# Optimization experiments

Hardware: AMD Instinct MI355X
Metric: run time of the kernel (lower is better)

## Reference

```python
import jax, jax.numpy as jnp
import numpy as np

N = 20000          # nodes
DEG = 8            # deterministic in-degree per node
E = N * DEG        # edges
IN_DIM = 16
HID = 128
EDGE_DIM = 8
OUT_DIM = 4
LN_EPS = 1e-5
# degree histogram has all mass at DEG -> avg log-degree = log(DEG + 1)
AVG_DEG_LOG = float(np.log(DEG + 1.0))


def _init(key, fan_in, fan_out):
    s = float(np.sqrt(2.0 / (fan_in + fan_out)))  # glorot-ish
    return jax.random.normal(key, (fan_in, fan_out), jnp.float32) * s


def setup_inputs() -> dict:
    key = jax.random.key(0)
    ks = jax.random.split(key, 24)
    x = jax.random.normal(ks[0], (N, IN_DIM), jnp.float32)
    src = jax.random.randint(ks[1], (E,), 0, N, jnp.int32)
    dst = (jnp.arange(E, dtype=jnp.int32) % N)  # every node has exactly DEG in-edges
    edge_index = jnp.stack([src, dst], axis=0)
    edge_attr = jax.random.normal(ks[2], (E, EDGE_DIM), jnp.float32)
    d = {"x": x, "edge_attr": edge_attr, "edge_index": edge_index}
    i = 3
    for l, fi in enumerate([IN_DIM, HID]):  # 2 PNAConv layers (num_layers=3)
        d[f"ew{l}"] = _init(ks[i], EDGE_DIM, fi); i += 1   # edge_encoder
        d[f"eb{l}"] = jnp.zeros((fi,), jnp.float32)
        d[f"pw{l}"] = _init(ks[i], 3 * fi, fi); i += 1     # pre_nn: cat(x_i,x_j,e)
        d[f"pb{l}"] = jnp.zeros((fi,), jnp.float32)
        d[f"qw{l}"] = _init(ks[i], 13 * fi, HID); i += 1   # post_nn: (4 aggr * 3 scalers + 1)*F_in
        d[f"qb{l}"] = jnp.zeros((HID,), jnp.float32)
        d[f"lw{l}"] = _init(ks[i], HID, HID); i += 1       # PNAConv.lin
        d[f"lb{l}"] = jnp.zeros((HID,), jnp.float32)
        d[f"g{l}"] = jnp.ones((HID,), jnp.float32)         # LayerNorm gamma
        d[f"b{l}"] = jnp.zeros((HID,), jnp.float32)        # LayerNorm beta
    d["hw"] = _init(ks[i], HID, OUT_DIM)
    d["hb"] = jnp.zeros((OUT_DIM,), jnp.float32)
    return d


def _pna_conv(x, src, dst, edge_attr, ew, eb, pw, pb, qw, qb, lw, lb):
    # messages: cat(x_i, x_j, edge_encoder(edge_attr)) -> pre MLP
    e = edge_attr @ ew + eb                                   # [E, F_in]
    h = jnp.concatenate([x[dst], x[src], e], axis=-1)         # [E, 3*F_in]
    h = h @ pw + pb                                           # [E, F_in]
    # multi-aggregator reduce by destination node
    deg = jax.ops.segment_sum(jnp.ones((E,), h.dtype), dst, num_segments=N)
    degc = jnp.maximum(deg, 1.0)[:, None]
    mean = jax.ops.segment_sum(h, dst, num_segments=N) / degc
    mean2 = jax.ops.segment_sum(h * h, dst, num_segments=N) / degc
    mx = jax.ops.segment_max(h, dst, num_segments=N)
    mn = jax.ops.segment_min(h, dst, num_segments=N)
    std = jnp.sqrt(jax.nn.relu(mean2 - mean * mean) + 1e-5)
    agg = jnp.concatenate([mean, mx, mn, std], axis=-1)       # [N, 4*F_in]
    # degree scalers: identity, amplification, attenuation (scaler-major layout)
    logd = jnp.log(deg + 1.0)[:, None]
    scaled = jnp.concatenate(
        [agg, agg * (logd / AVG_DEG_LOG), agg * (AVG_DEG_LOG / logd)], axis=-1
    )                                                         # [N, 12*F_in]
    out = jnp.concatenate([x, scaled], axis=-1) @ qw + qb     # post_nn, [N, F_out]
    return out @ lw + lb                                      # PNAConv.lin


def _ln(x, g, b):
    m = jnp.mean(x, axis=-1, keepdims=True)
    v = jnp.mean((x - m) ** 2, axis=-1, keepdims=True)
    return (x - m) / jnp.sqrt(v + LN_EPS) * g + b


def reference(x, edge_attr, ew0, eb0, pw0, pb0, qw0, qb0, lw0, lb0, g0, b0,
              ew1, eb1, pw1, pb1, qw1, qb1, lw1, lb1, g1, b1, hw, hb, edge_index):
    src, dst = edge_index[0], edge_index[1]
    h = _pna_conv(x, src, dst, edge_attr, ew0, eb0, pw0, pb0, qw0, qb0, lw0, lb0)
    h = jax.nn.relu(_ln(h, g0, b0))  # dropout is identity at inference
    h = _pna_conv(h, src, dst, edge_attr, ew1, eb1, pw1, pb1, qw1, qb1, lw1, lb1)
    h = jax.nn.relu(_ln(h, g1, b1))
    return h @ hw + hb               # head, [N, OUT_DIM]
```

## Files before the change

kernel.cpp:

```cpp
#include <hip/hip_runtime.h>
#include <math.h>

#define N_NODES 20000
#define N_EDGES 160000

typedef unsigned short ushort_t;
typedef __attribute__((ext_vector_type(8))) short short8v;
typedef __attribute__((ext_vector_type(4))) float f32x4;

#define WS_We0  0
#define WS_b0m  128
#define WS_W0   256
#define WS_b0   10496
#define WS_We1  10624
#define WS_b1m  11648
#define WS_W1   11776
#define WS_b1   93696
#define WS_WP1  93824
#define WS_WPTU 134784
#define WS_t0   151168
#define WS_u0   471168
#define WS_A0   791168
#define WS_A1   151168
#define WS_h0b  5271296
#define WS_t1   6551296
#define WS_u1   9111296

__device__ inline ushort_t f2bf(float f) {
    union { float f; unsigned u; } v; v.f = f;
    unsigned r = v.u + 0x7FFFu + ((v.u >> 16) & 1u);
    return (ushort_t)(r >> 16);
}

__global__ __launch_bounds__(256) void k_prep(
    const float* __restrict__ x,
    const float* __restrict__ ew0, const float* __restrict__ eb0,
    const float* __restrict__ pw0, const float* __restrict__ pb0,
    const float* __restrict__ qw0, const float* __restrict__ qb0,
    const float* __restrict__ lw0, const float* __restrict__ lb0,
    const float* __restrict__ ew1, const float* __restrict__ eb1,
    const float* __restrict__ pw1, const float* __restrict__ pb1,
    const float* __restrict__ qw1, const float* __restrict__ qb1,
    const float* __restrict__ lw1, const float* __restrict__ lb1,
    float* __restrict__ ws)
{
    int tid = blockIdx.x * 256 + threadIdx.x;
    if (tid < 81920) {
        int r = tid >> 7, o = tid & 127;
        float acc = 0.f;
        for (int h = 0; h < 128; ++h) {
            float qr;
            if (r < 128) qr = qw1[r*128 + h];
            else {
                int s = r - 128;
                qr = qw1[(128+s)*128+h] + qw1[(640+s)*128+h] + qw1[(1152+s)*128+h];
            }
            acc += qr * lw1[h*128 + o];
        }
        ws[WS_W1 + tid] = acc;
    } else if (tid < 82048) {
        int o = tid - 81920;
        float acc = lb1[o];
        for (int h = 0; h < 128; ++h) acc += qb1[h] * lw1[h*128 + o];
        ws[WS_b1 + o] = acc;
    } else if (tid < 92288) {
        int idx = tid - 82048; int r = idx >> 7, o = idx & 127;
        float acc = 0.f;
        for (int h = 0; h < 128; ++h) {
            float qr;
            if (r < 16) qr = qw0[r*128 + h];
            else {
                int s = r - 16;
                qr = qw0[(16+s)*128+h] + qw0[(80+s)*128+h] + qw0[(144+s)*128+h];
            }
            acc += qr * lw0[h*128 + o];
        }
        ws[WS_W0 + idx] = acc;
    } else if (tid < 92416) {
        int o = tid - 92288;
        float acc = lb0[o];
        for (int h = 0; h < 128; ++h) acc += qb0[h] * lw0[h*128 + o];
        ws[WS_b0 + o] = acc;
    } else if (tid < 93440) {
        int idx = tid - 92416; int c = idx >> 7, f = idx & 127;
        float acc = 0.f;
        for (int k = 0; k < 128; ++k) acc += ew1[c*128 + k] * pw1[(256+k)*128 + f];
        ws[WS_We1 + idx] = acc;
    } else if (tid < 93568) {
        int f = tid - 93440;
        float acc = pb1[f];
        for (int k = 0; k < 128; ++k) acc += eb1[k] * pw1[(256+k)*128 + f];
        ws[WS_b1m + f] = acc;
    } else if (tid < 93696) {
        int idx = tid - 93568; int c = idx >> 4, f = idx & 15;
        float acc = 0.f;
        for (int k = 0; k < 16; ++k) acc += ew0[c*16 + k] * pw0[(32+k)*16 + f];
        ws[WS_We0 + idx] = acc;
    } else if (tid < 93712) {
        int f = tid - 93696;
        float acc = pb0[f];
        for (int k = 0; k < 16; ++k) acc += eb0[k] * pw0[(32+k)*16 + f];
        ws[WS_b0m + f] = acc;
    } else if (tid < 413712) {
        int idx = tid - 93712; int i = idx >> 4, f = idx & 15;
        float acc = 0.f;
        for (int k = 0; k < 16; ++k) acc += x[i*16 + k] * pw0[k*16 + f];
        ws[WS_t0 + idx] = acc;
    } else if (tid < 733712) {
        int idx = tid - 413712; int i = idx >> 4, f = idx & 15;
        float acc = 0.f;
        for (int k = 0; k < 16; ++k) acc += x[i*16 + k] * pw0[(16+k)*16 + f];
        ws[WS_u0 + idx] = acc;
    }
}

__global__ __launch_bounds__(256) void k_pack(
    const float* __restrict__ pw1, float* __restrict__ ws)
{
    int tid = blockIdx.x * 256 + threadIdx.x;
    if (tid < 10240) {
        ushort_t* WP1 = (ushort_t*)(ws + WS_WP1);
        const float* W1f = ws + WS_W1;
        int l = tid & 63, ctks = tid >> 6;
        int ct = ctks / 20, ks = ctks % 20;
        int col = ct*16 + (l & 15);
        int k0 = ks*32 + (l >> 4)*8;
        short8v v;
        #pragma unroll
        for (int j = 0; j < 8; ++j) v[j] = (short)f2bf(W1f[(k0+j)*128 + col]);
        *(short8v*)(WP1 + (size_t)tid*8) = v;
    } else if (tid < 14336) {
        int idx = tid - 10240;
        ushort_t* WPT = (ushort_t*)(ws + WS_WPTU);
        int l = idx & 63, ctks = idx >> 6;
        int ct = ctks >> 2, ks = ctks & 3;
        int base_k = (ct < 8) ? 0 : 128;
        int col = (ct & 7)*16 + (l & 15);
        int k0 = base_k + ks*32 + (l >> 4)*8;
        short8v v;
        #pragma unroll
        for (int j = 0; j < 8; ++j) v[j] = (short)f2bf(pw1[(k0+j)*128 + col]);
        *(short8v*)(WPT + (size_t)idx*8) = v;
    }
}

__global__ __launch_bounds__(256) void k_agg0(
    const float* __restrict__ x, const float* __restrict__ ea,
    const int* __restrict__ src, float* __restrict__ ws)
{
    __shared__ float ea_s[16*8*8];
    __shared__ int   src_s[16*8];
    __shared__ float We0_s[128];
    __shared__ float b0m_s[16];
    const int t = threadIdx.x;
    const int i0 = blockIdx.x * 16;

    for (int idx = t; idx < 1024; idx += 256) {
        int k = idx >> 7; int rem = idx & 127; int n = rem >> 3, c = rem & 7;
        ea_s[(n*8 + k)*8 + c] = ea[(i0 + n + k*N_NODES)*8 + c];
    }
    if (t < 128) {
        int k = t >> 4, n = t & 15;
        src_s[n*8 + k] = src[i0 + n + k*N_NODES];
        We0_s[t] = ws[WS_We0 + t];
    }
    if (t < 16) b0m_s[t] = ws[WS_b0m + t];
    __syncthreads();

    const int n = t >> 4, f = t & 15;
    const int i = i0 + n;
    float base = ws[WS_t0 + i*16 + f] + b0m_s[f];
    float s = 0.f, q = 0.f, mx = -1e30f, mn = 1e30f;
    for (int k = 0; k < 8; ++k) {
        int sj = src_s[n*8 + k];
        float m = base + ws[WS_u0 + sj*16 + f];
        #pragma unroll
        for (int c = 0; c < 8; ++c) m += ea_s[(n*8+k)*8 + c] * We0_s[c*16 + f];
        s += m; q += m*m; mx = fmaxf(mx, m); mn = fminf(mn, m);
    }
    float mean = s * 0.125f, mean2 = q * 0.125f;
    float sd = sqrtf(fmaxf(mean2 - mean*mean, 0.f) + 1e-5f);
    float* A0 = ws + WS_A0 + (size_t)i * 80;
    A0[f]      = x[i*16 + f];
    A0[16 + f] = mean;
    A0[32 + f] = mx;
    A0[48 + f] = mn;
    A0[64 + f] = sd;
}

__global__ __launch_bounds__(256) void k_gemm0(
    const float* __restrict__ g0, const float* __restrict__ bln0,
    float* __restrict__ ws)
{
    __shared__ float As[32][81];
    const int t = threadIdx.x;
    const int r0 = blockIdx.x * 32;
    const float* A = ws + WS_A0 + (size_t)r0 * 80;
    for (int idx = t; idx < 32*80; idx += 256) {
        int r = idx / 80, k = idx - r*80;
        As[r][k] = A[idx];
    }
    __syncthreads();
    const int tc = t & 31, tr = t >> 5;
    const int c0 = tc * 4;
    float acc[4][4] = {};
    const float* W = ws + WS_W0;
    #pragma unroll 4
    for (int k = 0; k < 80; ++k) {
        float4 b = *(const float4*)(W + k*128 + c0);
        #pragma unroll
        for (int rr = 0; rr < 4; ++rr) {
            float a = As[tr*4 + rr][k];
            acc[rr][0] += a*b.x; acc[rr][1] += a*b.y;
            acc[rr][2] += a*b.z; acc[rr][3] += a*b.w;
        }
    }
    float4 bias = *(const float4*)(ws + WS_b0 + c0);
    float4 g  = *(const float4*)(g0 + c0);
    float4 bb = *(const float4*)(bln0 + c0);
    ushort_t* h0b = (ushort_t*)(ws + WS_h0b);
    #pragma unroll
    for (int rr = 0; rr < 4; ++rr) {
        float v0 = acc[rr][0] + bias.x, v1 = acc[rr][1] + bias.y;
        float v2 = acc[rr][2] + bias.z, v3 = acc[rr][3] + bias.w;
        float sum = v0+v1+v2+v3;
        float sq  = v0*v0+v1*v1+v2*v2+v3*v3;
        #pragma unroll
        for (int off = 1; off < 32; off <<= 1) {
            sum += __shfl_xor(sum, off, 64);
            sq  += __shfl_xor(sq,  off, 64);
        }
        float mean = sum * (1.f/128.f);
        float var  = sq  * (1.f/128.f) - mean*mean;
        float rstd = rsqrtf(var + 1e-5f);
        ushort4 ob;
        ob.x = f2bf(fmaxf((v0-mean)*rstd*g.x + bb.x, 0.f));
        ob.y = f2bf(fmaxf((v1-mean)*rstd*g.y + bb.y, 0.f));
        ob.z = f2bf(fmaxf((v2-mean)*rstd*g.z + bb.z, 0.f));
        ob.w = f2bf(fmaxf((v3-mean)*rstd*g.w + bb.w, 0.f));
        *(ushort4*)(h0b + (size_t)(r0 + tr*4 + rr)*128 + c0) = ob;
    }
}

__global__ __launch_bounds__(64) void k_tu1(float* __restrict__ ws)
{
    const int lane = threadIdx.x;
    const int rowbase = blockIdx.x * 16;
    const ushort_t* h0b = (const ushort_t*)(ws + WS_h0b);
    const ushort_t* WP  = (const ushort_t*)(ws + WS_WPTU);
    const int lr = lane & 15, lk = lane >> 4;
    const size_t arow = rowbase + lr;
    f32x4 acc[16];
    #pragma unroll
    for (int c = 0; c < 16; ++c) acc[c] = (f32x4){0.f,0.f,0.f,0.f};

    #pragma unroll
    for (int ks = 0; ks < 4; ++ks) {
        short8v a = *(const short8v*)(h0b + arow*128 + ks*32 + lk*8);
        #pragma unroll
        for (int c = 0; c < 16; ++c) {
            short8v b = *(const short8v*)(WP + ((size_t)(c*4 + ks)*64 + lane)*8);
            acc[c] = __builtin_amdgcn_mfma_f32_16x16x32_bf16(a, b, acc[c], 0, 0, 0);
        }
    }
    float* t1 = ws + WS_t1;
    float* u1 = ws + WS_u1;
    #pragma unroll
    for (int c = 0; c < 16; ++c) {
        float* dst = (c < 8) ? t1 : u1;
        int cb = (c & 7)*16 + lr;
        #pragma unroll
        for (int r = 0; r < 4; ++r) {
            int row = rowbase + lk*4 + r;
            dst[(size_t)row*128 + cb] = acc[c][r];
        }
    }
}

__global__ __launch_bounds__(256) void k_agg1(
    const float* __restrict__ ea, const int* __restrict__ src,
    float* __restrict__ ws)
{
    __shared__ float ea_s[16*8*8];
    __shared__ int   src_s[128];
    __shared__ float We1_s[1024];
    __shared__ float b1m_s[128];
    const int t = threadIdx.x;
    const int i0 = blockIdx.x * 16;

    for (int idx = t; idx < 1024; idx += 256) {
        int k = idx >> 7; int rem = idx & 127; int n = rem >> 3, c = rem & 7;
        ea_s[(n*8 + k)*8 + c] = ea[(i0 + n + k*N_NODES)*8 + c];
    }
    if (t < 128) {
        int k = t >> 4, n = t & 15;
        src_s[n*8 + k] = src[i0 + n + k*N_NODES];
    }
    for (int idx = t; idx < 1024; idx += 256) We1_s[idx] = ws[WS_We1 + idx];
    if (t < 128) b1m_s[t] = ws[WS_b1m + t];
    __syncthreads();

    const int n = t >> 4, f0 = (t & 15) * 8;
    const int i = i0 + n;
    float base[8], sm[8], sq[8], mx[8], mn[8];
    #pragma unroll
    for (int e = 0; e < 8; ++e) {
        base[e] = ws[WS_t1 + (size_t)i*128 + f0 + e] + b1m_s[f0 + e];
        sm[e] = 0.f; sq[e] = 0.f; mx[e] = -1e30f; mn[e] = 1e30f;
    }
    for (int k = 0; k < 8; ++k) {
        int sj = src_s[n*8 + k];
        const float* urow = ws + WS_u1 + (size_t)sj*128 + f0;
        float m[8];
        #pragma unroll
        for (int e = 0; e < 8; ++e) m[e] = base[e] + urow[e];
        #pragma unroll
        for (int c = 0; c < 8; ++c) {
            float a = ea_s[(n*8 + k)*8 + c];
            #pragma unroll
            for (int e = 0; e < 8; ++e) m[e] += a * We1_s[c*128 + f0 + e];
        }
        #pragma unroll
        for (int e = 0; e < 8; ++e) {
            sm[e] += m[e]; sq[e] += m[e]*m[e];
            mx[e] = fmaxf(mx[e], m[e]); mn[e] = fminf(mn[e], m[e]);
        }
    }
    ushort_t* A1 = (ushort_t*)(ws + WS_A1);
    short8v vm, vx, vn, vs;
    #pragma unroll
    for (int e = 0; e < 8; ++e) {
        float mean = sm[e]*0.125f, m2 = sq[e]*0.125f;
        float sd = sqrtf(fmaxf(m2 - mean*mean, 0.f) + 1e-5f);
        vm[e] = (short)f2bf(mean);
        vx[e] = (short)f2bf(mx[e]);
        vn[e] = (short)f2bf(mn[e]);
        vs[e] = (short)f2bf(sd);
    }
    size_t b = (size_t)i*512 + f0;
    *(short8v*)(A1 + b)       = vm;
    *(short8v*)(A1 + b + 128) = vx;
    *(short8v*)(A1 + b + 256) = vn;
    *(short8v*)(A1 + b + 384) = vs;
}

__global__ __launch_bounds__(64) void k_gemm1(
    const float* __restrict__ g1, const float* __restrict__ bln1,
    const float* __restrict__ hw, const float* __restrict__ hb,
    float* __restrict__ ws, float* __restrict__ out)
{
    const int lane = threadIdx.x;
    const int rowbase = blockIdx.x * 16;
    const ushort_t* h0b = (const ushort_t*)(ws + WS_h0b);
    const ushort_t* A1  = (const ushort_t*)(ws + WS_A1);
    const ushort_t* WP  = (const ushort_t*)(ws + WS_WP1);
    const int lr = lane & 15, lk = lane >> 4;
    const size_t arow = rowbase + lr;

    f32x4 acc[8];
    #pragma unroll
    for (int c = 0; c < 8; ++c) acc[c] = (f32x4){0.f,0.f,0.f,0.f};

    #pragma unroll
    for (int ks = 0; ks < 4; ++ks) {
        short8v a = *(const short8v*)(h0b + arow*128 + ks*32 + lk*8);
        #pragma unroll
        for (int c = 0; c < 8; ++c) {
            short8v b = *(const short8v*)(WP + ((size_t)(c*20 + ks)*64 + lane)*8);
            acc[c] = __builtin_amdgcn_mfma_f32_16x16x32_bf16(a, b, acc[c], 0, 0, 0);
        }
    }
    #pragma unroll 4
    for (int ks = 0; ks < 16; ++ks) {
        short8v a = *(const short8v*)(A1 + arow*512 + ks*32 + lk*8);
        #pragma unroll
        for (int c = 0; c < 8; ++c) {
            short8v b = *(const short8v*)(WP + ((size_t)(c*20 + 4 + ks)*64 + lane)*8);
            acc[c] = __builtin_amdgcn_mfma_f32_16x16x32_bf16(a, b, acc[c], 0, 0, 0);
        }
    }

    float bc[8], gc[8], bbc[8]; f32x4 hwc[8];
    #pragma unroll
    for (int c = 0; c < 8; ++c) {
        int col = c*16 + lr;
        bc[c]  = ws[WS_b1 + col];
        gc[c]  = g1[col];
        bbc[c] = bln1[col];
        hwc[c] = *(const f32x4*)(hw + col*4);
    }
    f32x4 hb4 = *(const f32x4*)hb;
    #pragma unroll
    for (int r = 0; r < 4; ++r) {
        float v[8]; float s = 0.f, q = 0.f;
        #pragma unroll
        for (int c = 0; c < 8; ++c) {
            v[c] = acc[c][r] + bc[c];
            s += v[c]; q += v[c]*v[c];
        }
        #pragma unroll
        for (int off = 1; off < 16; off <<= 1) {
            s += __shfl_xor(s, off, 64);
            q += __shfl_xor(q, off, 64);
        }
        float mean = s * (1.f/128.f);
        float var  = q * (1.f/128.f) - mean*mean;
        float rstd = rsqrtf(var + 1e-5f);
        f32x4 po = (f32x4){0.f,0.f,0.f,0.f};
        #pragma unroll
        for (int c = 0; c < 8; ++c) {
            float o = fmaxf((v[c]-mean)*rstd*gc[c] + bbc[c], 0.f);
            po += o * hwc[c];
        }
        #pragma unroll
        for (int off = 1; off < 16; off <<= 1) {
            po.x += __shfl_xor(po.x, off, 64);
            po.y += __shfl_xor(po.y, off, 64);
            po.z += __shfl_xor(po.z, off, 64);
            po.w += __shfl_xor(po.w, off, 64);
        }
        if (lr == 0) {
            int row = rowbase + lk*4 + r;
            f32x4 res = po + hb4;
            *(f32x4*)(out + (size_t)row*4) = res;
        }
    }
}

extern "C" void kernel_launch(void* const* d_in, const int* in_sizes, int n_in,
                              void* d_out, int out_size, void* d_ws, size_t ws_size,
                              hipStream_t stream)
{
    const float* x    = (const float*)d_in[0];
    const float* ea   = (const float*)d_in[1];
    const int*   eidx = (const int*)d_in[2];
    const float* ew0  = (const float*)d_in[3];
    const float* eb0  = (const float*)d_in[4];
    const float* pw0  = (const float*)d_in[5];
    const float* pb0  = (const float*)d_in[6];
    const float* qw0  = (const float*)d_in[7];
    const float* qb0  = (const float*)d_in[8];
    const float* lw0  = (const float*)d_in[9];
    const float* lb0  = (const float*)d_in[10];
    const float* g0   = (const float*)d_in[11];
    const float* bl0  = (const float*)d_in[12];
    const float* ew1  = (const float*)d_in[13];
    const float* eb1  = (const float*)d_in[14];
    const float* pw1  = (const float*)d_in[15];
    const float* pb1  = (const float*)d_in[16];
    const float* qw1  = (const float*)d_in[17];
    const float* qb1  = (const float*)d_in[18];
    const float* lw1  = (const float*)d_in[19];
    const float* lb1  = (const float*)d_in[20];
    const float* g1   = (const float*)d_in[21];
    const float* bl1  = (const float*)d_in[22];
    const float* hw   = (const float*)d_in[23];
    const float* hb   = (const float*)d_in[24];
    const int* src = eidx;
    float* ws = (float*)d_ws;
    float* out = (float*)d_out;

    k_prep<<<2867, 256, 0, stream>>>(x, ew0, eb0, pw0, pb0, qw0, qb0, lw0, lb0,
                                     ew1, eb1, pw1, pb1, qw1, qb1, lw1, lb1, ws);
    k_pack<<<56, 256, 0, stream>>>(pw1, ws);
    k_agg0<<<1250, 256, 0, stream>>>(x, ea, src, ws);
    k_gemm0<<<625, 256, 0, stream>>>(g0, bl0, ws);
    k_tu1<<<1250, 64, 0, stream>>>(ws);
    k_agg1<<<1250, 256, 0, stream>>>(ea, src, ws);
    k_gemm1<<<1250, 64, 0, stream>>>(g1, bl1, hw, hb, ws, out);
}
```

Baseline: 108.6 us.

## Fuse layer-1 aggregation into post-GEMM and pack weights directly in prep

The layer-1 aggregation kernel and the following MFMA GEMM kernel become one kernel. Each lane computes mean/max/min/std statistics for its row and feature slice in registers and feeds them straight into the MFMA A operands, so the bf16 aggregate buffer is never written to or read back from global memory. The separate weight-pack kernel is also removed: the prep kernel writes the bf16 MFMA-layout weights directly, which saves a launch and the fp32 intermediate. In exchange, each 64-thread block now does the gathers with lower parallelism and higher register pressure than the former 256-thread aggregation kernel.

```diff
diff --git a/kernel.cpp b/kernel.cpp
--- a/kernel.cpp
+++ b/kernel.cpp
@@ -7,6 +7,7 @@
 typedef unsigned short ushort_t;
 typedef __attribute__((ext_vector_type(8))) short short8v;
 typedef __attribute__((ext_vector_type(4))) float f32x4;
+typedef __attribute__((ext_vector_type(8))) float f32x8;
 
 #define WS_We0  0
 #define WS_b0m  128
@@ -14,17 +15,15 @@
 #define WS_b0   10496
 #define WS_We1  10624
 #define WS_b1m  11648
-#define WS_W1   11776
-#define WS_b1   93696
-#define WS_WP1  93824
-#define WS_WPTU 134784
-#define WS_t0   151168
-#define WS_u0   471168
-#define WS_A0   791168
-#define WS_A1   151168
-#define WS_h0b  5271296
-#define WS_t1   6551296
-#define WS_u1   9111296
+#define WS_b1   11776
+#define WS_WP1  11904
+#define WS_WPTU 52864
+#define WS_t0   69248
+#define WS_u0   389248
+#define WS_h0b  709248
+#define WS_t1   1989248
+#define WS_u1   4549248
+#define WS_A0   7109248
 
 __device__ inline ushort_t f2bf(float f) {
     union { float f; unsigned u; } v; v.f = f;
@@ -57,7 +56,9 @@
             }
             acc += qr * lw1[h*128 + o];
         }
-        ws[WS_W1 + tid] = acc;
+        int ct = o >> 4, ks = r >> 5;
+        int l = (o & 15) | (((r >> 3) & 3) << 4);
+        ((ushort_t*)(ws + WS_WP1))[(size_t)(((ct*20 + ks)*64) + l)*8 + (r & 7)] = f2bf(acc);
     } else if (tid < 82048) {
         int o = tid - 81920;
         float acc = lb1[o];
@@ -101,46 +102,24 @@
         float acc = pb0[f];
         for (int k = 0; k < 16; ++k) acc += eb0[k] * pw0[(32+k)*16 + f];
         ws[WS_b0m + f] = acc;
-    } else if (tid < 413712) {
-        int idx = tid - 93712; int i = idx >> 4, f = idx & 15;
+    } else if (tid < 126480) {
+        int idx = tid - 93712;
+        int r = idx >> 7, o = idx & 127;
+        int part = r >> 7, rk = r & 127;
+        int ct = part*8 + (o >> 4);
+        int l = (o & 15) | (((rk >> 3) & 3) << 4);
+        ((ushort_t*)(ws + WS_WPTU))[(size_t)(((ct*4 + (rk >> 5))*64) + l)*8 + (rk & 7)]
+            = f2bf(pw1[r*128 + o]);
+    } else if (tid < 446480) {
+        int idx = tid - 126480; int i = idx >> 4, f = idx & 15;
         float acc = 0.f;
         for (int k = 0; k < 16; ++k) acc += x[i*16 + k] * pw0[k*16 + f];
         ws[WS_t0 + idx] = acc;
-    } else if (tid < 733712) {
-        int idx = tid - 413712; int i = idx >> 4, f = idx & 15;
+    } else if (tid < 766480) {
+        int idx = tid - 446480; int i = idx >> 4, f = idx & 15;
         float acc = 0.f;
         for (int k = 0; k < 16; ++k) acc += x[i*16 + k] * pw0[(16+k)*16 + f];
         ws[WS_u0 + idx] = acc;
-    }
-}
-
-__global__ __launch_bounds__(256) void k_pack(
-    const float* __restrict__ pw1, float* __restrict__ ws)
-{
-    int tid = blockIdx.x * 256 + threadIdx.x;
-    if (tid < 10240) {
-        ushort_t* WP1 = (ushort_t*)(ws + WS_WP1);
-        const float* W1f = ws + WS_W1;
-        int l = tid & 63, ctks = tid >> 6;
-        int ct = ctks / 20, ks = ctks % 20;
-        int col = ct*16 + (l & 15);
-        int k0 = ks*32 + (l >> 4)*8;
-        short8v v;
-        #pragma unroll
-        for (int j = 0; j < 8; ++j) v[j] = (short)f2bf(W1f[(k0+j)*128 + col]);
-        *(short8v*)(WP1 + (size_t)tid*8) = v;
-    } else if (tid < 14336) {
-        int idx = tid - 10240;
-        ushort_t* WPT = (ushort_t*)(ws + WS_WPTU);
-        int l = idx & 63, ctks = idx >> 6;
-        int ct = ctks >> 2, ks = ctks & 3;
-        int base_k = (ct < 8) ? 0 : 128;
-        int col = (ct & 7)*16 + (l & 15);
-        int k0 = base_k + ks*32 + (l >> 4)*8;
-        short8v v;
-        #pragma unroll
-        for (int j = 0; j < 8; ++j) v[j] = (short)f2bf(pw1[(k0+j)*128 + col]);
-        *(short8v*)(WPT + (size_t)idx*8) = v;
     }
 }
 
@@ -277,106 +256,90 @@
     }
 }
 
-__global__ __launch_bounds__(256) void k_agg1(
+__global__ __launch_bounds__(64) void k_fuse1(
     const float* __restrict__ ea, const int* __restrict__ src,
-    float* __restrict__ ws)
-{
-    __shared__ float ea_s[16*8*8];
-    __shared__ int   src_s[128];
-    __shared__ float We1_s[1024];
-    __shared__ float b1m_s[128];
-    const int t = threadIdx.x;
-    const int i0 = blockIdx.x * 16;
-
-    for (int idx = t; idx < 1024; idx += 256) {
-        int k = idx >> 7; int rem = idx & 127; int n = rem >> 3, c = rem & 7;
-        ea_s[(n*8 + k)*8 + c] = ea[(i0 + n + k*N_NODES)*8 + c];
-    }
-    if (t < 128) {
-        int k = t >> 4, n = t & 15;
-        src_s[n*8 + k] = src[i0 + n + k*N_NODES];
-    }
-    for (int idx = t; idx < 1024; idx += 256) We1_s[idx] = ws[WS_We1 + idx];
-    if (t < 128) b1m_s[t] = ws[WS_b1m + t];
-    __syncthreads();
-
-    const int n = t >> 4, f0 = (t & 15) * 8;
-    const int i = i0 + n;
-    float base[8], sm[8], sq[8], mx[8], mn[8];
-    #pragma unroll
-    for (int e = 0; e < 8; ++e) {
-        base[e] = ws[WS_t1 + (size_t)i*128 + f0 + e] + b1m_s[f0 + e];
-        sm[e] = 0.f; sq[e] = 0.f; mx[e] = -1e30f; mn[e] = 1e30f;
-    }
-    for (int k = 0; k < 8; ++k) {
-        int sj = src_s[n*8 + k];
-        const float* urow = ws + WS_u1 + (size_t)sj*128 + f0;
-        float m[8];
-        #pragma unroll
-        for (int e = 0; e < 8; ++e) m[e] = base[e] + urow[e];
-        #pragma unroll
-        for (int c = 0; c < 8; ++c) {
-            float a = ea_s[(n*8 + k)*8 + c];
-            #pragma unroll
-            for (int e = 0; e < 8; ++e) m[e] += a * We1_s[c*128 + f0 + e];
-        }
-        #pragma unroll
-        for (int e = 0; e < 8; ++e) {
-            sm[e] += m[e]; sq[e] += m[e]*m[e];
-            mx[e] = fmaxf(mx[e], m[e]); mn[e] = fminf(mn[e], m[e]);
-        }
-    }
-    ushort_t* A1 = (ushort_t*)(ws + WS_A1);
-    short8v vm, vx, vn, vs;
-    #pragma unroll
-    for (int e = 0; e < 8; ++e) {
-        float mean = sm[e]*0.125f, m2 = sq[e]*0.125f;
-        float sd = sqrtf(fmaxf(m2 - mean*mean, 0.f) + 1e-5f);
-        vm[e] = (short)f2bf(mean);
-        vx[e] = (short)f2bf(mx[e]);
-        vn[e] = (short)f2bf(mn[e]);
-        vs[e] = (short)f2bf(sd);
-    }
-    size_t b = (size_t)i*512 + f0;
-    *(short8v*)(A1 + b)       = vm;
-    *(short8v*)(A1 + b + 128) = vx;
-    *(short8v*)(A1 + b + 256) = vn;
-    *(short8v*)(A1 + b + 384) = vs;
-}
-
-__global__ __launch_bounds__(64) void k_gemm1(
     const float* __restrict__ g1, const float* __restrict__ bln1,
     const float* __restrict__ hw, const float* __restrict__ hb,
     float* __restrict__ ws, float* __restrict__ out)
 {
     const int lane = threadIdx.x;
+    const int lr = lane & 15, lk = lane >> 4;
     const int rowbase = blockIdx.x * 16;
+    const int row = rowbase + lr;
     const ushort_t* h0b = (const ushort_t*)(ws + WS_h0b);
-    const ushort_t* A1  = (const ushort_t*)(ws + WS_A1);
     const ushort_t* WP  = (const ushort_t*)(ws + WS_WP1);
-    const int lr = lane & 15, lk = lane >> 4;
-    const size_t arow = rowbase + lr;
+
+    int sj[8];
+    #pragma unroll
+    for (int e = 0; e < 8; ++e) sj[e] = src[row + e*N_NODES];
 
     f32x4 acc[8];
     #pragma unroll
     for (int c = 0; c < 8; ++c) acc[c] = (f32x4){0.f,0.f,0.f,0.f};
 
     #pragma unroll
-    for (int ks = 0; ks < 4; ++ks) {
-        short8v a = *(const short8v*)(h0b + arow*128 + ks*32 + lk*8);
+    for (int kw = 0; kw < 4; ++kw) {
+        short8v a = *(const short8v*)(h0b + (size_t)row*128 + kw*32 + lk*8);
         #pragma unroll
         for (int c = 0; c < 8; ++c) {
-            short8v b = *(const short8v*)(WP + ((size_t)(c*20 + ks)*64 + lane)*8);
+            short8v b = *(const short8v*)(WP + (size_t)((c*20 + kw)*64 + lane)*8);
             acc[c] = __builtin_amdgcn_mfma_f32_16x16x32_bf16(a, b, acc[c], 0, 0, 0);
         }
     }
-    #pragma unroll 4
-    for (int ks = 0; ks < 16; ++ks) {
-        short8v a = *(const short8v*)(A1 + arow*512 + ks*32 + lk*8);
-        #pragma unroll
-        for (int c = 0; c < 8; ++c) {
-            short8v b = *(const short8v*)(WP + ((size_t)(c*20 + 4 + ks)*64 + lane)*8);
-            acc[c] = __builtin_amdgcn_mfma_f32_16x16x32_bf16(a, b, acc[c], 0, 0, 0);
+
+    #pragma unroll
+    for (int q = 0; q < 4; ++q) {
+        const int f0 = q*32 + lk*8;
+        f32x8 wv[8];
+        #pragma unroll
+        for (int c = 0; c < 8; ++c)
+            wv[c] = *(const f32x8*)(ws + WS_We1 + c*128 + f0);
+        f32x8 t1v  = *(const f32x8*)(ws + WS_t1 + (size_t)row*128 + f0);
+        f32x8 b1m8 = *(const f32x8*)(ws + WS_b1m + f0);
+        float base[8], sm[8], sq[8], mx[8], mn[8];
+        #pragma unroll
+        for (int j = 0; j < 8; ++j) {
+            base[j] = t1v[j] + b1m8[j];
+            sm[j] = 0.f; sq[j] = 0.f; mx[j] = -1e30f; mn[j] = 1e30f;
+        }
+        #pragma unroll
+        for (int e = 0; e < 8; ++e) {
+            f32x8 uv = *(const f32x8*)(ws + WS_u1 + (size_t)sj[e]*128 + f0);
+            f32x8 av = *(const f32x8*)(ea + (size_t)(row + e*N_NODES)*8);
+            float m[8];
+            #pragma unroll
+            for (int j = 0; j < 8; ++j) m[j] = base[j] + uv[j];
+            #pragma unroll
+            for (int c = 0; c < 8; ++c) {
+                #pragma unroll
+                for (int j = 0; j < 8; ++j) m[j] += av[c] * wv[c][j];
+            }
+            #pragma unroll
+            for (int j = 0; j < 8; ++j) {
+                sm[j] += m[j]; sq[j] += m[j]*m[j];
+                mx[j] = fmaxf(mx[j], m[j]); mn[j] = fminf(mn[j], m[j]);
+            }
+        }
+        float stat[4][8];
+        #pragma unroll
+        for (int j = 0; j < 8; ++j) {
+            float mean = sm[j]*0.125f, m2 = sq[j]*0.125f;
+            stat[0][j] = mean;
+            stat[1][j] = mx[j];
+            stat[2][j] = mn[j];
+            stat[3][j] = sqrtf(fmaxf(m2 - mean*mean, 0.f) + 1e-5f);
+        }
+        #pragma unroll
+        for (int agg = 0; agg < 4; ++agg) {
+            short8v a;
+            #pragma unroll
+            for (int j = 0; j < 8; ++j) a[j] = (short)f2bf(stat[agg][j]);
+            const int ks = agg*4 + q;
+            #pragma unroll
+            for (int c = 0; c < 8; ++c) {
+                short8v b = *(const short8v*)(WP + (size_t)((c*20 + 4 + ks)*64 + lane)*8);
+                acc[c] = __builtin_amdgcn_mfma_f32_16x16x32_bf16(a, b, acc[c], 0, 0, 0);
+            }
         }
     }
 
@@ -420,9 +383,8 @@
             po.w += __shfl_xor(po.w, off, 64);
         }
         if (lr == 0) {
-            int row = rowbase + lk*4 + r;
-            f32x4 res = po + hb4;
-            *(f32x4*)(out + (size_t)row*4) = res;
+            int orow = rowbase + lk*4 + r;
+            *(f32x4*)(out + (size_t)orow*4) = po + hb4;
         }
     }
 }
@@ -460,12 +422,10 @@
     float* ws = (float*)d_ws;
     float* out = (float*)d_out;
 
-    k_prep<<<2867, 256, 0, stream>>>(x, ew0, eb0, pw0, pb0, qw0, qb0, lw0, lb0,
+    k_prep<<<2995, 256, 0, stream>>>(x, ew0, eb0, pw0, pb0, qw0, qb0, lw0, lb0,
                                      ew1, eb1, pw1, pb1, qw1, qb1, lw1, lb1, ws);
-    k_pack<<<56, 256, 0, stream>>>(pw1, ws);
     k_agg0<<<1250, 256, 0, stream>>>(x, ea, src, ws);
     k_gemm0<<<625, 256, 0, stream>>>(g0, bl0, ws);
     k_tu1<<<1250, 64, 0, stream>>>(ws);
-    k_agg1<<<1250, 256, 0, stream>>>(ea, src, ws);
-    k_gemm1<<<1250, 64, 0, stream>>>(g1, bl1, hw, hb, ws, out);
-}
+    k_fuse1<<<1250, 64, 0, stream>>>(ea, src, g1, bl1, hw, hb, ws, out);
+}
```

Result: slower. 128.8 us (+18.7%).

## Fuse weight packing into prep kernel and split gemm1 columns across two waves

Applied to the files above, without the earlier changes.

The separate k_pack launch is removed: k_prep now writes the folded layer-1 weight and the packed pw1 tiles straight into the MFMA bf16 fragment layout, which saves a launch and the fp32 W1 intermediate buffer. k_gemm1 goes from one wave per 16-row tile to two waves, each computing half of the 128 output columns. LayerNorm statistics and head partial sums are combined through shared memory with two barriers. This lowers per-thread accumulator registers and doubles the waves in flight, at the cost of shared-memory reductions and synchronisation.

```diff
diff --git a/kernel.cpp b/kernel.cpp
--- a/kernel.cpp
+++ b/kernel.cpp
@@ -7,6 +7,7 @@
 typedef unsigned short ushort_t;
 typedef __attribute__((ext_vector_type(8))) short short8v;
 typedef __attribute__((ext_vector_type(4))) float f32x4;
+typedef __attribute__((ext_vector_type(8))) float f32x8;
 
 #define WS_We0  0
 #define WS_b0m  128
@@ -14,17 +15,16 @@
 #define WS_b0   10496
 #define WS_We1  10624
 #define WS_b1m  11648
-#define WS_W1   11776
-#define WS_b1   93696
-#define WS_WP1  93824
-#define WS_WPTU 134784
-#define WS_t0   151168
-#define WS_u0   471168
-#define WS_A0   791168
-#define WS_A1   151168
-#define WS_h0b  5271296
-#define WS_t1   6551296
-#define WS_u1   9111296
+#define WS_b1   11776
+#define WS_WP1  11904
+#define WS_WPTU 52864
+#define WS_t0   69248
+#define WS_u0   389248
+#define WS_h0b  709248
+#define WS_t1   1989248
+#define WS_u1   4549248
+#define WS_A0   7109248
+#define WS_A1   7109248
 
 __device__ inline ushort_t f2bf(float f) {
     union { float f; unsigned u; } v; v.f = f;
@@ -57,7 +57,9 @@
             }
             acc += qr * lw1[h*128 + o];
         }
-        ws[WS_W1 + tid] = acc;
+        int ct = o >> 4, ks = r >> 5;
+        int l = (o & 15) | (((r >> 3) & 3) << 4);
+        ((ushort_t*)(ws + WS_WP1))[(size_t)(((ct*20 + ks)*64) + l)*8 + (r & 7)] = f2bf(acc);
     } else if (tid < 82048) {
         int o = tid - 81920;
         float acc = lb1[o];
@@ -101,46 +103,24 @@
         float acc = pb0[f];
         for (int k = 0; k < 16; ++k) acc += eb0[k] * pw0[(32+k)*16 + f];
         ws[WS_b0m + f] = acc;
-    } else if (tid < 413712) {
-        int idx = tid - 93712; int i = idx >> 4, f = idx & 15;
+    } else if (tid < 126480) {
+        int idx = tid - 93712;
+        int r = idx >> 7, o = idx & 127;
+        int part = r >> 7, rk = r & 127;
+        int ct = part*8 + (o >> 4);
+        int l = (o & 15) | (((rk >> 3) & 3) << 4);
+        ((ushort_t*)(ws + WS_WPTU))[(size_t)(((ct*4 + (rk >> 5))*64) + l)*8 + (rk & 7)]
+            = f2bf(pw1[r*128 + o]);
+    } else if (tid < 446480) {
+        int idx = tid - 126480; int i = idx >> 4, f = idx & 15;
         float acc = 0.f;
         for (int k = 0; k < 16; ++k) acc += x[i*16 + k] * pw0[k*16 + f];
         ws[WS_t0 + idx] = acc;
-    } else if (tid < 733712) {
-        int idx = tid - 413712; int i = idx >> 4, f = idx & 15;
+    } else if (tid < 766480) {
+        int idx = tid - 446480; int i = idx >> 4, f = idx & 15;
         float acc = 0.f;
         for (int k = 0; k < 16; ++k) acc += x[i*16 + k] * pw0[(16+k)*16 + f];
         ws[WS_u0 + idx] = acc;
-    }
-}
-
-__global__ __launch_bounds__(256) void k_pack(
-    const float* __restrict__ pw1, float* __restrict__ ws)
-{
-    int tid = blockIdx.x * 256 + threadIdx.x;
-    if (tid < 10240) {
-        ushort_t* WP1 = (ushort_t*)(ws + WS_WP1);
-        const float* W1f = ws + WS_W1;
-        int l = tid & 63, ctks = tid >> 6;
-        int ct = ctks / 20, ks = ctks % 20;
-        int col = ct*16 + (l & 15);
-        int k0 = ks*32 + (l >> 4)*8;
-        short8v v;
-        #pragma unroll
-        for (int j = 0; j < 8; ++j) v[j] = (short)f2bf(W1f[(k0+j)*128 + col]);
-        *(short8v*)(WP1 + (size_t)tid*8) = v;
-    } else if (tid < 14336) {
-        int idx = tid - 10240;
-        ushort_t* WPT = (ushort_t*)(ws + WS_WPTU);
-        int l = idx & 63, ctks = idx >> 6;
-        int ct = ctks >> 2, ks = ctks & 3;
-        int base_k = (ct < 8) ? 0 : 128;
-        int col = (ct & 7)*16 + (l & 15);
-        int k0 = base_k + ks*32 + (l >> 4)*8;
-        short8v v;
-        #pragma unroll
-        for (int j = 0; j < 8; ++j) v[j] = (short)f2bf(pw1[(k0+j)*128 + col]);
-        *(short8v*)(WPT + (size_t)idx*8) = v;
     }
 }
 
@@ -344,72 +324,88 @@
     *(short8v*)(A1 + b + 384) = vs;
 }
 
-__global__ __launch_bounds__(64) void k_gemm1(
+__global__ __launch_bounds__(128) void k_gemm1(
     const float* __restrict__ g1, const float* __restrict__ bln1,
     const float* __restrict__ hw, const float* __restrict__ hb,
     float* __restrict__ ws, float* __restrict__ out)
 {
-    const int lane = threadIdx.x;
+    __shared__ float redS[2][16], redQ[2][16];
+    __shared__ f32x4 redP[16];
+    const int t = threadIdx.x;
+    const int w = t >> 6, lane = t & 63;
+    const int lr = lane & 15, lk = lane >> 4;
     const int rowbase = blockIdx.x * 16;
+    const int row = rowbase + lr;
     const ushort_t* h0b = (const ushort_t*)(ws + WS_h0b);
     const ushort_t* A1  = (const ushort_t*)(ws + WS_A1);
     const ushort_t* WP  = (const ushort_t*)(ws + WS_WP1);
-    const int lr = lane & 15, lk = lane >> 4;
-    const size_t arow = rowbase + lr;
-
-    f32x4 acc[8];
-    #pragma unroll
-    for (int c = 0; c < 8; ++c) acc[c] = (f32x4){0.f,0.f,0.f,0.f};
-
-    #pragma unroll
-    for (int ks = 0; ks < 4; ++ks) {
-        short8v a = *(const short8v*)(h0b + arow*128 + ks*32 + lk*8);
-        #pragma unroll
-        for (int c = 0; c < 8; ++c) {
-            short8v b = *(const short8v*)(WP + ((size_t)(c*20 + ks)*64 + lane)*8);
+
+    f32x4 acc[4];
+    #pragma unroll
+    for (int c = 0; c < 4; ++c) acc[c] = (f32x4){0.f,0.f,0.f,0.f};
+
+    #pragma unroll
+    for (int kw = 0; kw < 4; ++kw) {
+        short8v a = *(const short8v*)(h0b + (size_t)row*128 + kw*32 + lk*8);
+        #pragma unroll
+        for (int c = 0; c < 4; ++c) {
+            int ct = w*4 + c;
+            short8v b = *(const short8v*)(WP + (size_t)((ct*20 + kw)*64 + lane)*8);
             acc[c] = __builtin_amdgcn_mfma_f32_16x16x32_bf16(a, b, acc[c], 0, 0, 0);
         }
     }
     #pragma unroll 4
     for (int ks = 0; ks < 16; ++ks) {
-        short8v a = *(const short8v*)(A1 + arow*512 + ks*32 + lk*8);
-        #pragma unroll
-        for (int c = 0; c < 8; ++c) {
-            short8v b = *(const short8v*)(WP + ((size_t)(c*20 + 4 + ks)*64 + lane)*8);
+        short8v a = *(const short8v*)(A1 + (size_t)row*512 + ks*32 + lk*8);
+        #pragma unroll
+        for (int c = 0; c < 4; ++c) {
+            int ct = w*4 + c;
+            short8v b = *(const short8v*)(WP + (size_t)((ct*20 + 4 + ks)*64 + lane)*8);
             acc[c] = __builtin_amdgcn_mfma_f32_16x16x32_bf16(a, b, acc[c], 0, 0, 0);
         }
     }
 
-    float bc[8], gc[8], bbc[8]; f32x4 hwc[8];
-    #pragma unroll
-    for (int c = 0; c < 8; ++c) {
-        int col = c*16 + lr;
+    float bc[4], gc[4], bbc[4]; f32x4 hwc[4];
+    #pragma unroll
+    for (int c = 0; c < 4; ++c) {
+        int col = (w*4 + c)*16 + lr;
         bc[c]  = ws[WS_b1 + col];
         gc[c]  = g1[col];
         bbc[c] = bln1[col];
         hwc[c] = *(const f32x4*)(hw + col*4);
     }
-    f32x4 hb4 = *(const f32x4*)hb;
+
     #pragma unroll
     for (int r = 0; r < 4; ++r) {
-        float v[8]; float s = 0.f, q = 0.f;
-        #pragma unroll
-        for (int c = 0; c < 8; ++c) {
-            v[c] = acc[c][r] + bc[c];
-            s += v[c]; q += v[c]*v[c];
+        float s = 0.f, q = 0.f;
+        #pragma unroll
+        for (int c = 0; c < 4; ++c) {
+            float v = acc[c][r] + bc[c];
+            s += v; q += v*v;
         }
         #pragma unroll
         for (int off = 1; off < 16; off <<= 1) {
             s += __shfl_xor(s, off, 64);
             q += __shfl_xor(q, off, 64);
         }
-        float mean = s * (1.f/128.f);
-        float var  = q * (1.f/128.f) - mean*mean;
+        if (lr == 0) { redS[w][lk*4 + r] = s; redQ[w][lk*4 + r] = q; }
+    }
+    __syncthreads();
+
+    f32x4 poarr[4];
+    #pragma unroll
+    for (int r = 0; r < 4; ++r) {
+        int orow = lk*4 + r;
+        float s_tot = redS[0][orow] + redS[1][orow];
+        float q_tot = redQ[0][orow] + redQ[1][orow];
+        float mean = s_tot * (1.f/128.f);
+        float var  = q_tot * (1.f/128.f) - mean*mean;
         float rstd = rsqrtf(var + 1e-5f);
         f32x4 po = (f32x4){0.f,0.f,0.f,0.f};
         #pragma unroll
-        for (int c = 0; c < 8; ++c) {
-            float o = fmaxf((v[c]-mean)*rstd*gc[c] + bbc[c], 0.f);
+        for (int c = 0; c < 4; ++c) {
+            float v = acc[c][r] + bc[c];
+            float o = fmaxf((v-mean)*rstd*gc[c] + bbc[c], 0.f);
             po += o * hwc[c];
         }
         #pragma unroll
@@ -419,10 +415,18 @@
             po.z += __shfl_xor(po.z, off, 64);
             po.w += __shfl_xor(po.w, off, 64);
         }
-        if (lr == 0) {
-            int row = rowbase + lk*4 + r;
-            f32x4 res = po + hb4;
-            *(f32x4*)(out + (size_t)row*4) = res;
+        poarr[r] = po;
+        if (w == 1 && lr == 0) redP[orow] = po;
+    }
+    __syncthreads();
+
+    if (w == 0 && lr == 0) {
+        f32x4 hb4 = *(const f32x4*)hb;
+        #pragma unroll
+        for (int r = 0; r < 4; ++r) {
+            int orow = lk*4 + r;
+            f32x4 res = poarr[r] + redP[orow] + hb4;
+            *(f32x4*)(out + (size_t)(rowbase + orow)*4) = res;
         }
     }
 }
@@ -460,12 +464,11 @@
     float* ws = (float*)d_ws;
     float* out = (float*)d_out;
 
-    k_prep<<<2867, 256, 0, stream>>>(x, ew0, eb0, pw0, pb0, qw0, qb0, lw0, lb0,
+    k_prep<<<2995, 256, 0, stream>>>(x, ew0, eb0, pw0, pb0, qw0, qb0, lw0, lb0,
                                      ew1, eb1, pw1, pb1, qw1, qb1, lw1, lb1, ws);
-    k_pack<<<56, 256, 0, stream>>>(pw1, ws);
     k_agg0<<<1250, 256, 0, stream>>>(x, ea, src, ws);
     k_gemm0<<<625, 256, 0, stream>>>(g0, bl0, ws);
     k_tu1<<<1250, 64, 0, stream>>>(ws);
     k_agg1<<<1250, 256, 0, stream>>>(ea, src, ws);
-    k_gemm1<<<1250, 64, 0, stream>>>(g1, bl1, hw, hb, ws, out);
-}
+    k_gemm1<<<1250, 128, 0, stream>>>(g1, bl1, hw, hb, ws, out);
+}
```

Result: slower. 112.6 us (+3.7%).
